# Optimization experiments

Hardware: AMD Instinct MI355X
Metric: run time of the kernel (lower is better)

## Reference

```python
import jax, jax.numpy as jnp
import numpy as np

HEADS = 4
DIM_HEAD = 32
SCALE = 10.0  # scale=10 init arg
HIDDEN = HEADS * DIM_HEAD


def _l2norm(t, eps=1e-12):
    # matches torch F.normalize(t, dim=-1): normalize over last axis (flattened spatial)
    n = jnp.sqrt(jnp.sum(t * t, axis=-1, keepdims=True))
    return t / jnp.maximum(n, eps)


def setup_inputs() -> dict:
    key = jax.random.key(0)
    k1, k2, k3, k4, k5 = jax.random.split(key, 5)
    b, dim, H, W = 2, 128, 64, 64
    x = jax.random.normal(k1, (b, dim, H, W), jnp.float32)
    y = jax.random.normal(k2, (b, dim, H, W), jnp.float32)
    # to_qkv: Conv2d(dim, 3*hidden, 1, bias=False) -> weight (3*hidden, dim)
    w_qkv = jax.random.normal(k3, (3 * HIDDEN, dim), jnp.float32) / np.sqrt(dim)
    # to_out: Conv2d(hidden, dim, 1) -> weight (dim, hidden) + bias (dim,)
    w_out = jax.random.normal(k4, (dim, HIDDEN), jnp.float32) / np.sqrt(HIDDEN)
    b_out = jax.random.normal(k5, (dim,), jnp.float32) * 0.01
    return {"x": x, "y": y, "w_qkv": w_qkv, "w_out": w_out, "b_out": b_out}


def reference(x, y, w_qkv, w_out, b_out):
    b, c, H, W = x.shape
    n_x = H * W
    n_y = y.shape[2] * y.shape[3]
    xf = x.reshape(b, c, n_x)
    yf = y.reshape(b, c, n_y)
    # 1x1 conv == channel GEMM
    qkv_x = jnp.einsum('oc,bcn->bon', w_qkv, xf)
    qkv_y = jnp.einsum('oc,bcn->bon', w_qkv, yf)
    # only q from x, k/v from y are used downstream
    q_x = qkv_x[:, :HIDDEN].reshape(b, HEADS, DIM_HEAD, n_x)
    k_y = qkv_y[:, HIDDEN:2 * HIDDEN].reshape(b, HEADS, DIM_HEAD, n_y)
    v_y = qkv_y[:, 2 * HIDDEN:].reshape(b, HEADS, DIM_HEAD, n_y)
    q = _l2norm(q_x)
    k = _l2norm(k_y)
    sim = jnp.einsum('bhdi,bhdj->bhij', q, k) * SCALE  # [b,h,n_x,n_y]
    attn = jax.nn.softmax(sim, axis=-1)
    out = jnp.einsum('bhij,bhdj->bhdi', attn, v_y)  # [b,h,d,n_x]
    out = out.reshape(b, HIDDEN, H, W)  # 'b h (x y) d -> b (h d) x y'
    return jnp.einsum('oc,bcHW->boHW', w_out, out) + b_out[None, :, None, None]
```

## Files before the change

### kernel.cpp

```cpp
#include <hip/hip_runtime.h>
#include <hip/hip_bf16.h>

#define HEADS 4
#define DIMH  32
#define HID   128
#define DIM   128
#define NSP   4096
#define QSCALE_LOG2E 14.426950408889634f

typedef __attribute__((ext_vector_type(4)))  float f32x4;
typedef __attribute__((ext_vector_type(16))) float f32x16;
typedef __attribute__((ext_vector_type(8)))  short s16x8;

__device__ __forceinline__ unsigned cvtpk_bf16(float a, float b) {
  unsigned d;
  asm("v_cvt_pk_bf16_f32 %0, %1, %2" : "=v"(d) : "v"(a), "v"(b));
  return d;
}

__global__ __launch_bounds__(256) void k_cvt(const float* __restrict__ x,
                                             const float* __restrict__ y,
                                             __hip_bfloat16* __restrict__ xt,
                                             __hip_bfloat16* __restrict__ yt) {
  int bid = blockIdx.x;
  int t = bid >> 7, rem = bid & 127;
  int b = rem >> 6, nt = rem & 63;
  int n0 = nt * 64;
  const float* src = (t ? y : x) + (size_t)b * DIM * NSP;
  __hip_bfloat16* dst = (t ? yt : xt) + (size_t)b * NSP * DIM;

  __shared__ alignas(16) __hip_bfloat16 tile[64 * 136];
  int n = threadIdx.x & 63, c0 = threadIdx.x >> 6;
  const float* sp = src + n0 + n;
#pragma unroll
  for (int cc = 0; cc < 32; ++cc) {
    int c = cc * 4 + c0;
    tile[n * 136 + c] = __float2bfloat16(sp[(size_t)c * NSP]);
  }
  __syncthreads();
  int rrow = threadIdx.x >> 2, cb = (threadIdx.x & 3) * 32;
  __hip_bfloat16* op = dst + (size_t)(n0 + rrow) * DIM + cb;
  const __hip_bfloat16* ip = tile + rrow * 136 + cb;
#pragma unroll
  for (int k = 0; k < 4; ++k)
    *(s16x8*)(op + k * 8) = *(const s16x8*)(ip + k * 8);
}

__global__ __launch_bounds__(256, 4) void k_qkvm(const __hip_bfloat16* __restrict__ xt,
                                                 const __hip_bfloat16* __restrict__ yt,
                                                 const float* __restrict__ w,
                                                 float* __restrict__ ssp,
                                                 float* __restrict__ Qf,
                                                 __hip_bfloat16* __restrict__ Kr,
                                                 __hip_bfloat16* __restrict__ Vb) {
  int xcd = blockIdx.x & 7;
  int r = blockIdx.x >> 3;
  int ot = r >> 2;
  int nts = r & 3;
  int tile = xcd * 4 + nts;
  int n0 = tile * 256;
  int lane = threadIdx.x & 63, wave = threadIdx.x >> 6;
  int l31 = lane & 31, hi = lane >> 5;
  int orow = ot * 32 + l31;

  s16x8 wf[8];
  const float* wr = w + orow * DIM + hi * 8;
#pragma unroll
  for (int k = 0; k < 8; ++k) {
    f32x4 a = *(const f32x4*)(wr + k * 16);
    f32x4 b2 = *(const f32x4*)(wr + k * 16 + 4);
    union { unsigned u[4]; s16x8 v; } p;
    p.u[0] = cvtpk_bf16(a[0], a[1]);
    p.u[1] = cvtpk_bf16(a[2], a[3]);
    p.u[2] = cvtpk_bf16(b2[0], b2[1]);
    p.u[3] = cvtpk_bf16(b2[2], b2[3]);
    wf[k] = p.v;
  }

  const __hip_bfloat16* src = (ot < 4 ? xt : yt);
  int nw = n0 + wave * 64;
  f32x16 acc0 = {}, acc1 = {};
#pragma unroll
  for (int k = 0; k < 8; ++k) {
    s16x8 b0 = *(const s16x8*)(src + (size_t)(nw + l31) * DIM + k * 16 + hi * 8);
    s16x8 b1 = *(const s16x8*)(src + (size_t)(nw + 32 + l31) * DIM + k * 16 + hi * 8);
    acc0 = __builtin_amdgcn_mfma_f32_32x32x16_bf16(wf[k], b0, acc0, 0, 0, 0);
    acc1 = __builtin_amdgcn_mfma_f32_32x32x16_bf16(wf[k], b1, acc1, 0, 0, 0);
  }

  int b = nw >> 12;
  if (ot < 8) {
    int h = ot & 3;
    if (ot < 4) {
#pragma unroll
      for (int nt = 0; nt < 2; ++nt) {
        int np = (nw + nt * 32 + l31) & 4095;
        float* base = Qf + ((size_t)((b * HEADS + h) * NSP + np)) * DIMH;
        const f32x16& A = nt ? acc1 : acc0;
#pragma unroll
        for (int m = 0; m < 4; ++m) {
          f32x4 v = { A[4 * m], A[4 * m + 1], A[4 * m + 2], A[4 * m + 3] };
          *(f32x4*)(base + 8 * m + 4 * hi) = v;
        }
      }
    } else {
#pragma unroll
      for (int nt = 0; nt < 2; ++nt) {
        int np = (nw + nt * 32 + l31) & 4095;
        __hip_bfloat16* base = Kr + ((size_t)((b * HEADS + h) * NSP + np)) * DIMH;
        const f32x16& A = nt ? acc1 : acc0;
#pragma unroll
        for (int m = 0; m < 4; ++m) {
          uint2 p2;
          p2.x = cvtpk_bf16(A[4 * m], A[4 * m + 1]);
          p2.y = cvtpk_bf16(A[4 * m + 2], A[4 * m + 3]);
          *(uint2*)(base + 8 * m + 4 * hi) = p2;
        }
      }
    }
    float p[16];
#pragma unroll
    for (int r2 = 0; r2 < 16; ++r2) p[r2] = acc0[r2] * acc0[r2] + acc1[r2] * acc1[r2];
#pragma unroll
    for (int r2 = 0; r2 < 16; ++r2) {
#pragma unroll
      for (int m2 = 1; m2 < 32; m2 <<= 1) p[r2] += __shfl_xor(p[r2], m2);
    }
    if (l31 == 0) {
      int t = (ot < 4 ? 0 : 1);
      int widx = (tile & 15) * 4 + wave;
      int rbase = (t * 2 + b) * 128 + h * 32;
#pragma unroll
      for (int r2 = 0; r2 < 16; ++r2) {
        int row = (r2 & 3) + 8 * (r2 >> 2) + 4 * hi;
        ssp[(size_t)(rbase + row) * 64 + widx] = p[r2];
      }
    }
  } else {
    int h = ot - 8;
#pragma unroll
    for (int nt = 0; nt < 2; ++nt) {
      int np = (nw + nt * 32 + l31) & 4095;
      const f32x16& A = nt ? acc1 : acc0;
#pragma unroll
      for (int r2 = 0; r2 < 16; ++r2) {
        int d = (r2 & 3) + 8 * (r2 >> 2) + 4 * hi;
        Vb[((size_t)((b * HEADS + h) * DIMH + d)) * NSP + np] = __float2bfloat16(A[r2]);
      }
    }
  }
}

__global__ __launch_bounds__(512) void k_fac(const float* __restrict__ ssp,
                                             float* __restrict__ fsc) {
  int bh = blockIdx.x;
  int b = bh >> 2, h = bh & 3;
  int tid = threadIdx.x;
  int qk = tid >> 8, d = (tid >> 3) & 31, jj = tid & 7;
  const float* pp = ssp + (size_t)((qk * 2 + b) * 128 + h * 32 + d) * 64 + jj * 8;
  float s = 0.f;
#pragma unroll
  for (int k = 0; k < 8; ++k) s += pp[k];
  s += __shfl_down(s, 1); s += __shfl_down(s, 2); s += __shfl_down(s, 4);
  __shared__ float red[2][32];
  if (jj == 0) red[qk][d] = s;
  __syncthreads();
  if (tid < 32) {
    float vq = 1.f / fmaxf(sqrtf(red[0][tid]), 0.1f);
    float vk = 1.f / fmaxf(sqrtf(red[1][tid]), 0.1f);
    fsc[bh * 32 + tid] = vq * vk * QSCALE_LOG2E;
  }
}

__device__ __forceinline__ void glds16(const __hip_bfloat16* g, __hip_bfloat16* l) {
  __builtin_amdgcn_global_load_lds(
      (const __attribute__((address_space(1))) unsigned int*)(const void*)g,
      (__attribute__((address_space(3))) unsigned int*)(void*)l, 16, 0, 0);
}

__device__ __forceinline__ void attn_sub2(const __hip_bfloat16* kbase,
                                          const __hip_bfloat16* vbase,
                                          int s, int l31, int hi,
                                          s16x8 qb0, s16x8 qb1,
                                          f32x16& O, float& lsum) {
  int krx = l31 & 3, vrx = l31 & 7;
  const __hip_bfloat16* krow = kbase + (s * 32 + l31) * DIMH;
  s16x8 kf0 = *(const s16x8*)(krow + (((hi) ^ krx) << 3));
  s16x8 kf1 = *(const s16x8*)(krow + (((2 + hi) ^ krx) << 3));
  f32x16 z = {};
  f32x16 sv = __builtin_amdgcn_mfma_f32_32x32x16_bf16(kf0, qb0, z, 0, 0, 0);
  sv        = __builtin_amdgcn_mfma_f32_32x32x16_bf16(kf1, qb1, sv, 0, 0, 0);
  float p[16];
#pragma unroll
  for (int r = 0; r < 16; ++r) p[r] = __builtin_amdgcn_exp2f(sv[r]);
  float t0 = 0.f, t1 = 0.f;
#pragma unroll
  for (int r = 0; r < 16; r += 2) { t0 += p[r]; t1 += p[r + 1]; }
  lsum += t0 + t1;
  unsigned wA[4], wB[4];
#pragma unroll
  for (int m = 0; m < 4; ++m) {
    wA[m] = cvtpk_bf16(p[4 * m], p[4 * m + 1]);
    wB[m] = cvtpk_bf16(p[4 * m + 2], p[4 * m + 3]);
  }
  const __hip_bfloat16* vrow = vbase + l31 * 64;
#define PV_CHUNK(c2, vfrag)                                                    \
  {                                                                            \
    unsigned a0 = wA[2 * (c2)], a1 = wA[2 * (c2) + 1];                         \
    unsigned b0 = wB[2 * (c2)], b1 = wB[2 * (c2) + 1];                         \
    asm("v_permlane32_swap_b32 %0, %1" : "+v"(a0), "+v"(a1));                  \
    asm("v_permlane32_swap_b32 %0, %1" : "+v"(b0), "+v"(b1));                  \
    union { unsigned u[4]; s16x8 v; } pa;                                      \
    pa.u[0] = a0; pa.u[1] = b0; pa.u[2] = a1; pa.u[3] = b1;                    \
    O = __builtin_amdgcn_mfma_f32_32x32x16_bf16(pa.v, vfrag, O, 0, 0, 0);      \
  }
#pragma unroll
  for (int c2 = 0; c2 < 2; ++c2) {
    int cc = s * 2 + c2;
    s16x8 vf = *(const s16x8*)(vrow + (((cc * 2 + hi) ^ vrx) << 3));
    PV_CHUNK(c2, vf);
  }
#undef PV_CHUNK
}

__global__ __launch_bounds__(1024, 4) void k_attn(const float* __restrict__ Qf,
                                                  const __hip_bfloat16* __restrict__ Kt,
                                                  const __hip_bfloat16* __restrict__ Vb,
                                                  const float* __restrict__ fsc,
                                                  __hip_bfloat16* __restrict__ Otb) {
  int bh = blockIdx.x & 7, qt = blockIdx.x >> 3;
  int tid = threadIdx.x, lane = tid & 63, wave = tid >> 6;
  int qsub = wave & 3, jq = wave >> 2;
  int l31 = lane & 31, hi = lane >> 5;
  int i0 = qt * 128 + qsub * 32;
  int jbase = jq * 1024;

  __shared__ alignas(16) char smem[65536];
  __shared__ float Llds[16][64];
  __hip_bfloat16* KsB = (__hip_bfloat16*)smem;
  __hip_bfloat16* VsB = KsB + 16384;
  float* Olds = (float*)smem;

  const __hip_bfloat16* kg = Kt + (size_t)bh * NSP * DIMH;
  const __hip_bfloat16* vg = Vb + (size_t)bh * DIMH * NSP;

  const float* qpf = Qf + ((size_t)bh * NSP + i0 + l31) * DIMH;
  const float* fb = fsc + bh * 32;
  s16x8 qb0, qb1;
  {
    f32x4 a0 = *(const f32x4*)(qpf + hi * 8);
    f32x4 a1 = *(const f32x4*)(qpf + hi * 8 + 4);
    f32x4 a2 = *(const f32x4*)(qpf + 16 + hi * 8);
    f32x4 a3 = *(const f32x4*)(qpf + 16 + hi * 8 + 4);
    f32x4 f0 = *(const f32x4*)(fb + hi * 8);
    f32x4 f1 = *(const f32x4*)(fb + hi * 8 + 4);
    f32x4 f2 = *(const f32x4*)(fb + 16 + hi * 8);
    f32x4 f3 = *(const f32x4*)(fb + 16 + hi * 8 + 4);
    union { unsigned u[4]; s16x8 v; } p0, p1;
    p0.u[0] = cvtpk_bf16(a0[0] * f0[0], a0[1] * f0[1]);
    p0.u[1] = cvtpk_bf16(a0[2] * f0[2], a0[3] * f0[3]);
    p0.u[2] = cvtpk_bf16(a1[0] * f1[0], a1[1] * f1[1]);
    p0.u[3] = cvtpk_bf16(a1[2] * f1[2], a1[3] * f1[3]);
    p1.u[0] = cvtpk_bf16(a2[0] * f2[0], a2[1] * f2[1]);
    p1.u[1] = cvtpk_bf16(a2[2] * f2[2], a2[3] * f2[3]);
    p1.u[2] = cvtpk_bf16(a3[0] * f3[0], a3[1] * f3[1]);
    p1.u[3] = cvtpk_bf16(a3[2] * f3[2], a3[3] * f3[3]);
    qb0 = p0.v; qb1 = p1.v;
  }

  int ku = qsub * 64 + lane;
  int krow = ku >> 2;
  int kchunk = (ku & 3) ^ (krow & 3);
  const __hip_bfloat16* ksrc0 = kg + (size_t)krow * DIMH + (kchunk << 3);
  int vd = ku >> 3;
  int vchunk = (ku & 7) ^ (vd & 7);
  const __hip_bfloat16* vsrc0 = vg + (size_t)vd * NSP + (vchunk << 3);
  int lbase = qsub * 512;

  f32x16 O = {};
  float ls0 = 0.f, ls1 = 0.f;

  glds16(ksrc0 + (size_t)jbase * DIMH, &KsB[(jq * 2 + 0) * 2048 + lbase]);
  glds16(vsrc0 + jbase,                &VsB[(jq * 2 + 0) * 2048 + lbase]);
  asm volatile("s_waitcnt vmcnt(0)" ::: "memory");
  __syncthreads();

#pragma unroll 1
  for (int t = 0; t < 16; ++t) {
    int buf = t & 1;
    if (t < 15) {
      int j1 = jbase + (t + 1) * 64;
      glds16(ksrc0 + (size_t)j1 * DIMH, &KsB[(jq * 2 + (buf ^ 1)) * 2048 + lbase]);
      glds16(vsrc0 + j1,                &VsB[(jq * 2 + (buf ^ 1)) * 2048 + lbase]);
    }
    const __hip_bfloat16* kbase = &KsB[(jq * 2 + buf) * 2048];
    const __hip_bfloat16* vbase = &VsB[(jq * 2 + buf) * 2048];
    attn_sub2(kbase, vbase, 0, l31, hi, qb0, qb1, O, ls0);
    attn_sub2(kbase, vbase, 1, l31, hi, qb0, qb1, O, ls1);
    if (t < 15) {
      asm volatile("s_waitcnt vmcnt(0)" ::: "memory");
      __syncthreads();
    }
  }

  float lsum = ls0 + ls1;
  float lw = lsum + __shfl_xor(lsum, 32);
  Llds[wave][lane] = lw;
  __syncthreads();
  if (jq) {
    float* od = Olds + (size_t)(qsub * 3 + (jq - 1)) * 1088;
#pragma unroll
    for (int r = 0; r < 16; ++r) od[r * 68 + lane] = O[r];
  }
  __syncthreads();
  if (jq == 0) {
    float ltot = lw + Llds[wave + 4][lane] + Llds[wave + 8][lane] + Llds[wave + 12][lane];
    if (hi == 0) Llds[wave][l31] = ltot;
    float* o0 = Olds + (size_t)(qsub * 3) * 1088;
    float* o1 = o0 + 1088;
    float* o2 = o1 + 1088;
#pragma unroll
    for (int r = 0; r < 16; ++r) {
      int i = (r & 3) + 8 * (r >> 2) + 4 * hi;
      float li = Llds[wave][i];
      float sum = O[r] + o0[r * 68 + lane] + o1[r * 68 + lane] + o2[r * 68 + lane];
      o0[r * 68 + lane] = sum / li;
    }
  }
  __syncthreads();
  {
    int q2 = tid >> 8;
    int i  = (tid >> 3) & 31;
    int cp = tid & 7;
    int r  = (i & 3) | ((i >> 3) << 2);
    int h2 = (i >> 2) & 1;
    const float* o0 = Olds + (size_t)(q2 * 3) * 1088 + r * 68 + h2 * 32 + cp * 4;
    uint2 pv;
    pv.x = cvtpk_bf16(o0[0], o0[1]);
    pv.y = cvtpk_bf16(o0[2], o0[3]);
    int b2 = bh >> 2, h = bh & 3;
    __hip_bfloat16* dst = Otb + ((size_t)(b2 * NSP + qt * 128 + q2 * 32 + i)) * HID + h * 32 + cp * 4;
    *(uint2*)dst = pv;
  }
}

__global__ __launch_bounds__(256, 4) void k_projm(const __hip_bfloat16* __restrict__ Otb,
                                                  const float* __restrict__ w,
                                                  const float* __restrict__ bias,
                                                  float* __restrict__ out) {
  int xcd = blockIdx.x & 7;
  int ot  = (blockIdx.x >> 3) & 3;
  int yy  = blockIdx.x >> 5;
  int tile = xcd * 8 + yy;
  int n0 = tile * 128;
  int lane = threadIdx.x & 63, wave = threadIdx.x >> 6;
  int l31 = lane & 31, hi = lane >> 5;
  int orow = ot * 32 + l31;

  s16x8 wf[8];
  const float* wr = w + orow * HID + hi * 8;
#pragma unroll
  for (int k = 0; k < 8; ++k) {
    f32x4 a = *(const f32x4*)(wr + k * 16);
    f32x4 b2 = *(const f32x4*)(wr + k * 16 + 4);
    union { unsigned u[4]; s16x8 v; } p;
    p.u[0] = cvtpk_bf16(a[0], a[1]);
    p.u[1] = cvtpk_bf16(a[2], a[3]);
    p.u[2] = cvtpk_bf16(b2[0], b2[1]);
    p.u[3] = cvtpk_bf16(b2[2], b2[3]);
    wf[k] = p.v;
  }

  int nw = n0 + wave * 32;
  int b = nw >> 12, np = nw & 4095;
  const __hip_bfloat16* src = Otb + ((size_t)(b * NSP + np)) * HID;
  f32x16 acc = {};
#pragma unroll
  for (int k = 0; k < 8; ++k) {
    s16x8 bfr = *(const s16x8*)(src + (size_t)l31 * HID + k * 16 + hi * 8);
    acc = __builtin_amdgcn_mfma_f32_32x32x16_bf16(wf[k], bfr, acc, 0, 0, 0);
  }

  float* outb = out + (size_t)b * DIM * NSP + np + l31;
#pragma unroll
  for (int r2 = 0; r2 < 16; ++r2) {
    int o = ot * 32 + (r2 & 3) + 8 * (r2 >> 2) + 4 * hi;
    outb[(size_t)o * NSP] = acc[r2] + bias[o];
  }
}

extern "C" void kernel_launch(void* const* d_in, const int* in_sizes, int n_in,
                              void* d_out, int out_size, void* d_ws, size_t ws_size,
                              hipStream_t stream) {
  const float* x     = (const float*)d_in[0];
  const float* y     = (const float*)d_in[1];
  const float* w_qkv = (const float*)d_in[2];
  const float* w_out = (const float*)d_in[3];
  const float* b_out = (const float*)d_in[4];
  float* out = (float*)d_out;

  char* ws = (char*)d_ws;
  __hip_bfloat16* xt  = (__hip_bfloat16*)(ws);
  __hip_bfloat16* yt  = (__hip_bfloat16*)(ws + (2  << 20));
  float* Qf           = (float*)(ws + (4  << 20));
  __hip_bfloat16* Kr  = (__hip_bfloat16*)(ws + (8  << 20));
  __hip_bfloat16* Vb  = (__hip_bfloat16*)(ws + (10 << 20));
  __hip_bfloat16* Otb = (__hip_bfloat16*)(ws + (12 << 20));
  float* ssp          = (float*)(ws + (16 << 20));
  float* fsc          = (float*)(ws + (16 << 20) + (128 << 10));

  k_cvt   <<<256,  256,  0, stream>>>(x, y, xt, yt);
  k_qkvm  <<<384,  256,  0, stream>>>(xt, yt, w_qkv, ssp, Qf, Kr, Vb);
  k_fac   <<<8,    512,  0, stream>>>(ssp, fsc);
  k_attn  <<<256,  1024, 0, stream>>>(Qf, Kr, Vb, fsc, Otb);
  k_projm <<<256,  256,  0, stream>>>(Otb, w_out, b_out, out);
}
```

Measured before the change: 60.90 us.

## Shrink attention blocks to per-wave private K/V pipelines and fold norm factors in

Restructures the attention kernel from 1024-thread blocks sharing double-buffered 64-key tiles behind block barriers into 256-thread blocks where each wave streams its own 32-key tiles into private LDS buffers, synchronised only through vmcnt waits, with no __syncthreads in the main loop. The separate k_fac launch is removed and each attention block recomputes the q/k normalisation factors from ssp itself. s_setprio is raised around the MFMA instructions. The aim is to cut barrier stalls and one kernel launch, at the cost of redundant factor reduction in every block and a four-times larger grid.

```diff
diff --git a/kernel.cpp b/kernel.cpp
--- a/kernel.cpp
+++ b/kernel.cpp
@@ -151,45 +151,26 @@
   }
 }
 
-__global__ __launch_bounds__(512) void k_fac(const float* __restrict__ ssp,
-                                             float* __restrict__ fsc) {
-  int bh = blockIdx.x;
-  int b = bh >> 2, h = bh & 3;
-  int tid = threadIdx.x;
-  int qk = tid >> 8, d = (tid >> 3) & 31, jj = tid & 7;
-  const float* pp = ssp + (size_t)((qk * 2 + b) * 128 + h * 32 + d) * 64 + jj * 8;
-  float s = 0.f;
-#pragma unroll
-  for (int k = 0; k < 8; ++k) s += pp[k];
-  s += __shfl_down(s, 1); s += __shfl_down(s, 2); s += __shfl_down(s, 4);
-  __shared__ float red[2][32];
-  if (jj == 0) red[qk][d] = s;
-  __syncthreads();
-  if (tid < 32) {
-    float vq = 1.f / fmaxf(sqrtf(red[0][tid]), 0.1f);
-    float vk = 1.f / fmaxf(sqrtf(red[1][tid]), 0.1f);
-    fsc[bh * 32 + tid] = vq * vk * QSCALE_LOG2E;
-  }
-}
-
 __device__ __forceinline__ void glds16(const __hip_bfloat16* g, __hip_bfloat16* l) {
   __builtin_amdgcn_global_load_lds(
       (const __attribute__((address_space(1))) unsigned int*)(const void*)g,
       (__attribute__((address_space(3))) unsigned int*)(void*)l, 16, 0, 0);
 }
 
-__device__ __forceinline__ void attn_sub2(const __hip_bfloat16* kbase,
+__device__ __forceinline__ void attn_sub3(const __hip_bfloat16* kbase,
                                           const __hip_bfloat16* vbase,
-                                          int s, int l31, int hi,
+                                          int l31, int hi,
                                           s16x8 qb0, s16x8 qb1,
                                           f32x16& O, float& lsum) {
-  int krx = l31 & 3, vrx = l31 & 7;
-  const __hip_bfloat16* krow = kbase + (s * 32 + l31) * DIMH;
-  s16x8 kf0 = *(const s16x8*)(krow + (((hi) ^ krx) << 3));
-  s16x8 kf1 = *(const s16x8*)(krow + (((2 + hi) ^ krx) << 3));
+  int rx = l31 & 3;
+  const __hip_bfloat16* krow = kbase + l31 * DIMH;
+  s16x8 kf0 = *(const s16x8*)(krow + (((hi) ^ rx) << 3));
+  s16x8 kf1 = *(const s16x8*)(krow + (((2 + hi) ^ rx) << 3));
   f32x16 z = {};
+  __builtin_amdgcn_s_setprio(1);
   f32x16 sv = __builtin_amdgcn_mfma_f32_32x32x16_bf16(kf0, qb0, z, 0, 0, 0);
   sv        = __builtin_amdgcn_mfma_f32_32x32x16_bf16(kf1, qb1, sv, 0, 0, 0);
+  __builtin_amdgcn_s_setprio(0);
   float p[16];
 #pragma unroll
   for (int r = 0; r < 16; ++r) p[r] = __builtin_amdgcn_exp2f(sv[r]);
@@ -203,7 +184,7 @@
     wA[m] = cvtpk_bf16(p[4 * m], p[4 * m + 1]);
     wB[m] = cvtpk_bf16(p[4 * m + 2], p[4 * m + 3]);
   }
-  const __hip_bfloat16* vrow = vbase + l31 * 64;
+  const __hip_bfloat16* vrow = vbase + l31 * 32;
 #define PV_CHUNK(c2, vfrag)                                                    \
   {                                                                            \
     unsigned a0 = wA[2 * (c2)], a1 = wA[2 * (c2) + 1];                         \
@@ -212,50 +193,71 @@
     asm("v_permlane32_swap_b32 %0, %1" : "+v"(b0), "+v"(b1));                  \
     union { unsigned u[4]; s16x8 v; } pa;                                      \
     pa.u[0] = a0; pa.u[1] = b0; pa.u[2] = a1; pa.u[3] = b1;                    \
+    __builtin_amdgcn_s_setprio(1);                                             \
     O = __builtin_amdgcn_mfma_f32_32x32x16_bf16(pa.v, vfrag, O, 0, 0, 0);      \
+    __builtin_amdgcn_s_setprio(0);                                             \
   }
 #pragma unroll
   for (int c2 = 0; c2 < 2; ++c2) {
-    int cc = s * 2 + c2;
-    s16x8 vf = *(const s16x8*)(vrow + (((cc * 2 + hi) ^ vrx) << 3));
+    s16x8 vf = *(const s16x8*)(vrow + (((c2 * 2 + hi) ^ rx) << 3));
     PV_CHUNK(c2, vf);
   }
 #undef PV_CHUNK
 }
 
-__global__ __launch_bounds__(1024, 4) void k_attn(const float* __restrict__ Qf,
-                                                  const __hip_bfloat16* __restrict__ Kt,
-                                                  const __hip_bfloat16* __restrict__ Vb,
-                                                  const float* __restrict__ fsc,
-                                                  __hip_bfloat16* __restrict__ Otb) {
+__global__ __launch_bounds__(256, 4) void k_attn(const float* __restrict__ Qf,
+                                                 const __hip_bfloat16* __restrict__ Kt,
+                                                 const __hip_bfloat16* __restrict__ Vb,
+                                                 const float* __restrict__ ssp,
+                                                 __hip_bfloat16* __restrict__ Otb) {
   int bh = blockIdx.x & 7, qt = blockIdx.x >> 3;
   int tid = threadIdx.x, lane = tid & 63, wave = tid >> 6;
-  int qsub = wave & 3, jq = wave >> 2;
   int l31 = lane & 31, hi = lane >> 5;
-  int i0 = qt * 128 + qsub * 32;
-  int jbase = jq * 1024;
-
-  __shared__ alignas(16) char smem[65536];
-  __shared__ float Llds[16][64];
+  int i0 = qt * 32;
+  int jbase = wave * 1024;
+  int b = bh >> 2, h = bh & 3;
+
+  __shared__ alignas(16) char smem[32768];
+  __shared__ float Llds[4][64];
+  __shared__ float redl[64];
+  __shared__ float fscl[32];
   __hip_bfloat16* KsB = (__hip_bfloat16*)smem;
-  __hip_bfloat16* VsB = KsB + 16384;
+  __hip_bfloat16* VsB = KsB + 8192;
   float* Olds = (float*)smem;
+
+  {
+    int row = tid >> 2, part = tid & 3;
+    int qk = row >> 5, r32 = row & 31;
+    const float* pp = ssp + (size_t)((qk * 2 + b) * 128 + h * 32 + r32) * 64 + part * 16;
+    float s = 0.f;
+#pragma unroll
+    for (int k = 0; k < 16; ++k) s += pp[k];
+    s += __shfl_xor(s, 1);
+    s += __shfl_xor(s, 2);
+    if (part == 0) redl[row] = s;
+  }
+  __syncthreads();
+  if (tid < 32) {
+    float vq = 1.f / fmaxf(sqrtf(redl[tid]), 0.1f);
+    float vk = 1.f / fmaxf(sqrtf(redl[tid + 32]), 0.1f);
+    fscl[tid] = vq * vk * QSCALE_LOG2E;
+  }
+  __syncthreads();
 
   const __hip_bfloat16* kg = Kt + (size_t)bh * NSP * DIMH;
   const __hip_bfloat16* vg = Vb + (size_t)bh * DIMH * NSP;
 
   const float* qpf = Qf + ((size_t)bh * NSP + i0 + l31) * DIMH;
-  const float* fb = fsc + bh * 32;
   s16x8 qb0, qb1;
   {
     f32x4 a0 = *(const f32x4*)(qpf + hi * 8);
     f32x4 a1 = *(const f32x4*)(qpf + hi * 8 + 4);
     f32x4 a2 = *(const f32x4*)(qpf + 16 + hi * 8);
     f32x4 a3 = *(const f32x4*)(qpf + 16 + hi * 8 + 4);
-    f32x4 f0 = *(const f32x4*)(fb + hi * 8);
-    f32x4 f1 = *(const f32x4*)(fb + hi * 8 + 4);
-    f32x4 f2 = *(const f32x4*)(fb + 16 + hi * 8);
-    f32x4 f3 = *(const f32x4*)(fb + 16 + hi * 8 + 4);
+    f32x4 f0 = *(const f32x4*)(fscl + hi * 8);
+    f32x4 f1 = *(const f32x4*)(fscl + hi * 8 + 4);
+    f32x4 f2 = *(const f32x4*)(fscl + 16 + hi * 8);
+    f32x4 f3 = *(const f32x4*)(fscl + 16 + hi * 8 + 4);
     union { unsigned u[4]; s16x8 v; } p0, p1;
     p0.u[0] = cvtpk_bf16(a0[0] * f0[0], a0[1] * f0[1]);
     p0.u[1] = cvtpk_bf16(a0[2] * f0[2], a0[3] * f0[3]);
@@ -268,78 +270,78 @@
     qb0 = p0.v; qb1 = p1.v;
   }
 
-  int ku = qsub * 64 + lane;
-  int krow = ku >> 2;
-  int kchunk = (ku & 3) ^ (krow & 3);
-  const __hip_bfloat16* ksrc0 = kg + (size_t)krow * DIMH + (kchunk << 3);
-  int vd = ku >> 3;
-  int vchunk = (ku & 7) ^ (vd & 7);
-  const __hip_bfloat16* vsrc0 = vg + (size_t)vd * NSP + (vchunk << 3);
-  int lbase = qsub * 512;
+  int rw = lane >> 2;
+  int ch = (lane & 3) ^ (rw & 3);
+  const __hip_bfloat16* ksA = kg + (size_t)rw * DIMH + (ch << 3);
+  const __hip_bfloat16* ksB2 = ksA + 16 * DIMH;
+  const __hip_bfloat16* vsA = vg + (size_t)rw * NSP + (ch << 3);
+  const __hip_bfloat16* vsB2 = vsA + 16 * NSP;
+  __hip_bfloat16* kd0 = KsB + wave * 2048;
+  __hip_bfloat16* vd0 = VsB + wave * 2048;
 
   f32x16 O = {};
   float ls0 = 0.f, ls1 = 0.f;
 
-  glds16(ksrc0 + (size_t)jbase * DIMH, &KsB[(jq * 2 + 0) * 2048 + lbase]);
-  glds16(vsrc0 + jbase,                &VsB[(jq * 2 + 0) * 2048 + lbase]);
-  asm volatile("s_waitcnt vmcnt(0)" ::: "memory");
-  __syncthreads();
-
+#define STAGE(j0, buf)                                                         \
+  {                                                                            \
+    glds16(ksA  + (size_t)(j0) * DIMH, kd0 + (buf) * 1024);                    \
+    glds16(ksB2 + (size_t)(j0) * DIMH, kd0 + (buf) * 1024 + 512);              \
+    glds16(vsA  + (j0), vd0 + (buf) * 1024);                                   \
+    glds16(vsB2 + (j0), vd0 + (buf) * 1024 + 512);                             \
+  }
+
+  STAGE(jbase, 0);
 #pragma unroll 1
-  for (int t = 0; t < 16; ++t) {
-    int buf = t & 1;
-    if (t < 15) {
-      int j1 = jbase + (t + 1) * 64;
-      glds16(ksrc0 + (size_t)j1 * DIMH, &KsB[(jq * 2 + (buf ^ 1)) * 2048 + lbase]);
-      glds16(vsrc0 + j1,                &VsB[(jq * 2 + (buf ^ 1)) * 2048 + lbase]);
-    }
-    const __hip_bfloat16* kbase = &KsB[(jq * 2 + buf) * 2048];
-    const __hip_bfloat16* vbase = &VsB[(jq * 2 + buf) * 2048];
-    attn_sub2(kbase, vbase, 0, l31, hi, qb0, qb1, O, ls0);
-    attn_sub2(kbase, vbase, 1, l31, hi, qb0, qb1, O, ls1);
-    if (t < 15) {
+  for (int tt = 0; tt < 16; ++tt) {
+    int t0 = tt * 2;
+    STAGE(jbase + (t0 + 1) * 32, 1);
+    asm volatile("s_waitcnt vmcnt(4)" ::: "memory");
+    attn_sub3(kd0, vd0, l31, hi, qb0, qb1, O, ls0);
+    if (tt < 15) {
+      STAGE(jbase + (t0 + 2) * 32, 0);
+      asm volatile("s_waitcnt vmcnt(4)" ::: "memory");
+    } else {
       asm volatile("s_waitcnt vmcnt(0)" ::: "memory");
-      __syncthreads();
-    }
-  }
+    }
+    attn_sub3(kd0 + 1024, vd0 + 1024, l31, hi, qb0, qb1, O, ls1);
+  }
+#undef STAGE
 
   float lsum = ls0 + ls1;
   float lw = lsum + __shfl_xor(lsum, 32);
   Llds[wave][lane] = lw;
   __syncthreads();
-  if (jq) {
-    float* od = Olds + (size_t)(qsub * 3 + (jq - 1)) * 1088;
+  if (wave) {
+    float* od = Olds + (size_t)(wave - 1) * 1088;
 #pragma unroll
     for (int r = 0; r < 16; ++r) od[r * 68 + lane] = O[r];
   }
   __syncthreads();
-  if (jq == 0) {
-    float ltot = lw + Llds[wave + 4][lane] + Llds[wave + 8][lane] + Llds[wave + 12][lane];
-    if (hi == 0) Llds[wave][l31] = ltot;
-    float* o0 = Olds + (size_t)(qsub * 3) * 1088;
+  if (wave == 0) {
+    float ltot = lw + Llds[1][lane] + Llds[2][lane] + Llds[3][lane];
+    if (hi == 0) Llds[0][l31] = ltot;
+    float* o0 = Olds;
     float* o1 = o0 + 1088;
     float* o2 = o1 + 1088;
 #pragma unroll
     for (int r = 0; r < 16; ++r) {
       int i = (r & 3) + 8 * (r >> 2) + 4 * hi;
-      float li = Llds[wave][i];
+      float li = Llds[0][i];
       float sum = O[r] + o0[r * 68 + lane] + o1[r * 68 + lane] + o2[r * 68 + lane];
       o0[r * 68 + lane] = sum / li;
     }
   }
   __syncthreads();
   {
-    int q2 = tid >> 8;
     int i  = (tid >> 3) & 31;
     int cp = tid & 7;
     int r  = (i & 3) | ((i >> 3) << 2);
     int h2 = (i >> 2) & 1;
-    const float* o0 = Olds + (size_t)(q2 * 3) * 1088 + r * 68 + h2 * 32 + cp * 4;
+    const float* o0 = Olds + r * 68 + h2 * 32 + cp * 4;
     uint2 pv;
     pv.x = cvtpk_bf16(o0[0], o0[1]);
     pv.y = cvtpk_bf16(o0[2], o0[3]);
-    int b2 = bh >> 2, h = bh & 3;
-    __hip_bfloat16* dst = Otb + ((size_t)(b2 * NSP + qt * 128 + q2 * 32 + i)) * HID + h * 32 + cp * 4;
+    __hip_bfloat16* dst = Otb + ((size_t)(b * NSP + i0 + i)) * HID + h * 32 + cp * 4;
     *(uint2*)dst = pv;
   }
 }
@@ -407,11 +409,9 @@
   __hip_bfloat16* Vb  = (__hip_bfloat16*)(ws + (10 << 20));
   __hip_bfloat16* Otb = (__hip_bfloat16*)(ws + (12 << 20));
   float* ssp          = (float*)(ws + (16 << 20));
-  float* fsc          = (float*)(ws + (16 << 20) + (128 << 10));
-
-  k_cvt   <<<256,  256,  0, stream>>>(x, y, xt, yt);
-  k_qkvm  <<<384,  256,  0, stream>>>(xt, yt, w_qkv, ssp, Qf, Kr, Vb);
-  k_fac   <<<8,    512,  0, stream>>>(ssp, fsc);
-  k_attn  <<<256,  1024, 0, stream>>>(Qf, Kr, Vb, fsc, Otb);
-  k_projm <<<256,  256,  0, stream>>>(Otb, w_out, b_out, out);
-}
+
+  k_cvt   <<<256,  256, 0, stream>>>(x, y, xt, yt);
+  k_qkvm  <<<384,  256, 0, stream>>>(xt, yt, w_qkv, ssp, Qf, Kr, Vb);
+  k_attn  <<<1024, 256, 0, stream>>>(Qf, Kr, Vb, ssp, Otb);
+  k_projm <<<256,  256, 0, stream>>>(Otb, w_out, b_out, out);
+}
```

After: 62.85 us. 1.03x slower.
